# Kernel tuning notes

Measured on AMD Instinct MI355X. Metric: run time of the kernel, lower is better.

Reference implementation:

```python
import jax, jax.numpy as jnp
import numpy as np

N_NODES = 100000
N_EDGES = 3200000
NFEAT = 512
NCLASS = 10


def setup_inputs() -> dict:
    key = jax.random.key(0)
    ks = jax.random.split(key, 8)
    x = jax.random.normal(ks[0], (N_NODES, NFEAT), dtype=jnp.float32)
    edge_index = jax.random.randint(ks[1], (2, N_EDGES), 0, N_NODES, dtype=jnp.int64)
    edge_weight = jax.random.uniform(ks[2], (N_EDGES,), dtype=jnp.float32)
    def glorot(k, fan_in, fan_out):
        s = jnp.sqrt(2.0 / (fan_in + fan_out)).astype(jnp.float32)
        return jax.random.normal(k, (fan_in, fan_out), dtype=jnp.float32) * s
    W1 = glorot(ks[3], NFEAT, 8)
    W2 = glorot(ks[4], 8, 16)
    W3 = glorot(ks[5], 16, 8)
    W4 = glorot(ks[6], 8, NCLASS)
    return {
        "x": x, "edge_index": edge_index, "edge_weight": edge_weight,
        "W1": W1, "b1": jnp.zeros((8,), jnp.float32),
        "W2": W2, "b2": jnp.zeros((16,), jnp.float32),
        "W3": W3, "b3": jnp.zeros((8,), jnp.float32),
        "W4": W4, "b4": jnp.zeros((NCLASS,), jnp.float32),
    }


def gcn_conv(x, W, b, src, dst, w):
    # standard Kipf GCNConv: out = A @ (x @ W) + b, A given as weighted edge list
    h = x @ W                                   # [N, F_out]  (tiny F_out)
    msg = h[src] * w[:, None]                   # gather + scale  [E, F_out]
    agg = jax.ops.segment_sum(msg, dst, num_segments=x.shape[0])
    return agg + b


def reference(x, edge_index, edge_weight, W1, b1, W2, b2, W3, b3, W4, b4):
    src, dst = edge_index[0], edge_index[1]
    # dropout is a no-op in eval mode (training=False)
    h = jax.nn.relu(gcn_conv(x, W1, b1, src, dst, edge_weight))
    h = jax.nn.relu(gcn_conv(h, W2, b2, src, dst, edge_weight))
    h = jax.nn.relu(gcn_conv(h, W3, b3, src, dst, edge_weight))
    h = gcn_conv(h, W4, b4, src, dst, edge_weight)
    return jax.nn.log_softmax(h, axis=1)
```

## Files before the change

### kernel.cpp

```cpp
#include <hip/hip_runtime.h>
#include <hip/hip_bf16.h>
#include <math.h>

#define NFEAT 512
#define SCAN_BS 256

__global__ __launch_bounds__(256) void gcn_mm512x8(
    const float* __restrict__ x, const float* __restrict__ W,
    float* __restrict__ out, int N)
{
  const int lane   = threadIdx.x & 63;
  const int wid    = blockIdx.x * (blockDim.x >> 6) + (threadIdx.x >> 6);
  const int nwaves = gridDim.x * (blockDim.x >> 6);

  float Wr[8][8];
  #pragma unroll
  for (int k = 0; k < 8; ++k) {
    const float4 wa = *reinterpret_cast<const float4*>(W + (size_t)(lane*8 + k)*8);
    const float4 wb = *reinterpret_cast<const float4*>(W + (size_t)(lane*8 + k)*8 + 4);
    Wr[k][0]=wa.x; Wr[k][1]=wa.y; Wr[k][2]=wa.z; Wr[k][3]=wa.w;
    Wr[k][4]=wb.x; Wr[k][5]=wb.y; Wr[k][6]=wb.z; Wr[k][7]=wb.w;
  }

  for (int n = wid; n < N; n += nwaves) {
    const float* xr = x + (size_t)n * NFEAT + lane*8;
    const float4 a0 = *reinterpret_cast<const float4*>(xr);
    const float4 a1 = *reinterpret_cast<const float4*>(xr + 4);
    const float a[8] = {a0.x,a0.y,a0.z,a0.w,a1.x,a1.y,a1.z,a1.w};
    float acc[8] = {0.f,0.f,0.f,0.f,0.f,0.f,0.f,0.f};
    #pragma unroll
    for (int k = 0; k < 8; ++k)
      #pragma unroll
      for (int o = 0; o < 8; ++o)
        acc[o] = fmaf(a[k], Wr[k][o], acc[o]);
    #pragma unroll
    for (int o = 0; o < 8; ++o) {
      float v = acc[o];
      v += __shfl_xor(v, 32, 64); v += __shfl_xor(v, 16, 64);
      v += __shfl_xor(v,  8, 64); v += __shfl_xor(v,  4, 64);
      v += __shfl_xor(v,  2, 64); v += __shfl_xor(v,  1, 64);
      acc[o] = v;
    }
    if (lane == 0) {
      float4* op = reinterpret_cast<float4*>(out + (size_t)n*8);
      op[0] = make_float4(acc[0],acc[1],acc[2],acc[3]);
      op[1] = make_float4(acc[4],acc[5],acc[6],acc[7]);
    }
  }
}

__global__ __launch_bounds__(256) void gcn_hist_rank(
    const int* __restrict__ dst, int* __restrict__ deg,
    int* __restrict__ rank, int E)
{
  const int e = blockIdx.x * blockDim.x + threadIdx.x;
  if (e < E) rank[e] = atomicAdd(&deg[dst[e]], 1);
}

__global__ __launch_bounds__(SCAN_BS) void gcn_scan_block(
    const int* __restrict__ deg, int* __restrict__ exc,
    int* __restrict__ bsums, int N)
{
  __shared__ int sm[SCAN_BS];
  const int i = blockIdx.x * SCAN_BS + threadIdx.x;
  const int v = (i < N) ? deg[i] : 0;
  sm[threadIdx.x] = v;
  __syncthreads();
  for (int off = 1; off < SCAN_BS; off <<= 1) {
    const int t = (threadIdx.x >= off) ? sm[threadIdx.x - off] : 0;
    __syncthreads();
    sm[threadIdx.x] += t;
    __syncthreads();
  }
  if (i < N) exc[i] = sm[threadIdx.x] - v;
  if (threadIdx.x == SCAN_BS-1) bsums[blockIdx.x] = sm[threadIdx.x];
}

__global__ __launch_bounds__(1024) void gcn_scan_bsums(int* __restrict__ bsums, int NB)
{
  __shared__ int sm[1024];
  const int t = threadIdx.x;
  const int v = (t < NB) ? bsums[t] : 0;
  sm[t] = v;
  __syncthreads();
  for (int off = 1; off < 1024; off <<= 1) {
    const int u = (t >= off) ? sm[t - off] : 0;
    __syncthreads();
    sm[t] += u;
    __syncthreads();
  }
  if (t < NB) bsums[t] = sm[t] - v;
}

__global__ __launch_bounds__(SCAN_BS) void gcn_scan_add(
    int* __restrict__ exc, const int* __restrict__ bsums, int N)
{
  const int i = blockIdx.x * SCAN_BS + threadIdx.x;
  if (i < N) exc[i] += bsums[blockIdx.x];
}

__global__ __launch_bounds__(256) void gcn_csr_scatter(
    const int* __restrict__ src, const int* __restrict__ dst,
    const float* __restrict__ w, const int* __restrict__ rowoff,
    const int* __restrict__ rank, int2* __restrict__ csr, int E)
{
  const int e = blockIdx.x * blockDim.x + threadIdx.x;
  if (e >= E) return;
  const int pos = rowoff[dst[e]] + rank[e];
  const unsigned long long payload =
      (unsigned long long)(unsigned)src[e] |
      ((unsigned long long)(unsigned)__float_as_int(w[e]) << 32);
  __builtin_nontemporal_store(payload, (unsigned long long*)&csr[pos]);
}

template<int FIN, int FOUT>
__global__ __launch_bounds__(256) void gcn_agg_layer(
    const int* __restrict__ rowoff, const int2* __restrict__ csr,
    const float* __restrict__ hin,
    const float* __restrict__ bias, const float* __restrict__ W,
    float* __restrict__ hout, int N, int E)
{
  const int sub = threadIdx.x & 15;
  const int n   = (blockIdx.x * blockDim.x + threadIdx.x) >> 4;
  if (n >= N) return;
  const int beg = rowoff[n];
  const int end = (n + 1 < N) ? rowoff[n + 1] : E;

  float acc[FIN];
  #pragma unroll
  for (int k = 0; k < FIN; ++k) acc[k] = 0.f;

  for (int e = beg + sub; e < end; e += 16) {
    const int2  sw = csr[e];
    const float wt = __int_as_float(sw.y);
    const float* hp = hin + (size_t)sw.x * FIN;
    if constexpr ((FIN & 3) == 0) {
      #pragma unroll
      for (int q = 0; q < FIN/4; ++q) {
        const float4 v = reinterpret_cast<const float4*>(hp)[q];
        acc[q*4+0] = fmaf(v.x, wt, acc[q*4+0]);
        acc[q*4+1] = fmaf(v.y, wt, acc[q*4+1]);
        acc[q*4+2] = fmaf(v.z, wt, acc[q*4+2]);
        acc[q*4+3] = fmaf(v.w, wt, acc[q*4+3]);
      }
    } else {
      #pragma unroll
      for (int q = 0; q < FIN/2; ++q) {
        const float2 v = reinterpret_cast<const float2*>(hp)[q];
        acc[q*2+0] = fmaf(v.x, wt, acc[q*2+0]);
        acc[q*2+1] = fmaf(v.y, wt, acc[q*2+1]);
      }
    }
  }
  #pragma unroll
  for (int k = 0; k < FIN; ++k) {
    float v = acc[k];
    v += __shfl_xor(v, 8, 64); v += __shfl_xor(v, 4, 64);
    v += __shfl_xor(v, 2, 64); v += __shfl_xor(v, 1, 64);
    acc[k] = v;
  }
  #pragma unroll
  for (int k = 0; k < FIN; ++k) {
    const float t = acc[k] + bias[k];
    acc[k] = t > 0.f ? t : 0.f;
  }
  if (sub < FOUT) {
    float o = 0.f;
    #pragma unroll
    for (int k = 0; k < FIN; ++k)
      o = fmaf(acc[k], W[k*FOUT + sub], o);
    hout[(size_t)n*FOUT + sub] = o;
  }
}

__global__ __launch_bounds__(256) void gcn_agg_final(
    const int* __restrict__ rowoff, const int2* __restrict__ csr,
    const float* __restrict__ hin,
    const float* __restrict__ bias, float* __restrict__ out, int N, int E)
{
  const int sub = threadIdx.x & 15;
  const int n   = (blockIdx.x * blockDim.x + threadIdx.x) >> 4;
  if (n >= N) return;
  const int beg = rowoff[n];
  const int end = (n + 1 < N) ? rowoff[n + 1] : E;

  float acc[10];
  #pragma unroll
  for (int k = 0; k < 10; ++k) acc[k] = 0.f;

  for (int e = beg + sub; e < end; e += 16) {
    const int2  sw = csr[e];
    const float wt = __int_as_float(sw.y);
    const float* hp = hin + (size_t)sw.x * 10;
    #pragma unroll
    for (int q = 0; q < 5; ++q) {
      const float2 v = reinterpret_cast<const float2*>(hp)[q];
      acc[q*2+0] = fmaf(v.x, wt, acc[q*2+0]);
      acc[q*2+1] = fmaf(v.y, wt, acc[q*2+1]);
    }
  }
  #pragma unroll
  for (int k = 0; k < 10; ++k) {
    float v = acc[k];
    v += __shfl_xor(v, 8, 64); v += __shfl_xor(v, 4, 64);
    v += __shfl_xor(v, 2, 64); v += __shfl_xor(v, 1, 64);
    acc[k] = v + bias[k];
  }
  float m = acc[0];
  #pragma unroll
  for (int k = 1; k < 10; ++k) m = fmaxf(m, acc[k]);
  float s = 0.f;
  #pragma unroll
  for (int k = 0; k < 10; ++k) s += expf(acc[k] - m);
  const float ls = logf(s) + m;
  if (sub < 10)
    out[(size_t)n*10 + sub] = acc[sub] - ls;
}

extern "C" void kernel_launch(void* const* d_in, const int* in_sizes, int n_in,
                              void* d_out, int out_size, void* d_ws, size_t ws_size,
                              hipStream_t stream)
{
  const float* x  = (const float*)d_in[0];
  const int*   ei = (const int*)  d_in[1];
  const float* ew = (const float*)d_in[2];
  const float* W1 = (const float*)d_in[3];
  const float* b1 = (const float*)d_in[4];
  const float* W2 = (const float*)d_in[5];
  const float* b2 = (const float*)d_in[6];
  const float* W3 = (const float*)d_in[7];
  const float* b3 = (const float*)d_in[8];
  const float* W4 = (const float*)d_in[9];
  const float* b4 = (const float*)d_in[10];

  const int N = in_sizes[0] / NFEAT;
  const int E = in_sizes[2];
  const int* src = ei;
  const int* dst = ei + E;

  const int NB = (N + SCAN_BS - 1) / SCAN_BS;

  int*   wsp    = (int*)d_ws;
  int*   deg    = wsp;
  int*   rowoff = wsp + N;
  int*   bsums  = wsp + 2*(size_t)N;
  int*   rank   = wsp + 2*(size_t)N + 1024;
  int2*  csr    = (int2*)(rank + E);
  float* h8     = (float*)(csr + E);
  float* h16    = h8 + (size_t)N*8;
  float* h10    = h16;
  float* outp   = (float*)d_out;

  const int eb   = (E + 255) / 256;
  const int nb16 = (N*16 + 255) / 256;

  hipMemsetAsync(deg, 0, (size_t)N*sizeof(int), stream);
  gcn_hist_rank<<<eb, 256, 0, stream>>>(dst, deg, rank, E);
  gcn_scan_block<<<NB, SCAN_BS, 0, stream>>>(deg, rowoff, bsums, N);
  gcn_scan_bsums<<<1, 1024, 0, stream>>>(bsums, NB);
  gcn_scan_add<<<NB, SCAN_BS, 0, stream>>>(rowoff, bsums, N);
  gcn_csr_scatter<<<eb, 256, 0, stream>>>(src, dst, ew, rowoff, rank, csr, E);

  gcn_mm512x8<<<2048, 256, 0, stream>>>(x, W1, h8, N);

  gcn_agg_layer<8,16><<<nb16, 256, 0, stream>>>(rowoff, csr, h8,  b1, W2, h16, N, E);
  gcn_agg_layer<16,8><<<nb16, 256, 0, stream>>>(rowoff, csr, h16, b2, W3, h8,  N, E);
  gcn_agg_layer<8,10><<<nb16, 256, 0, stream>>>(rowoff, csr, h8,  b3, W4, h10, N, E);
  gcn_agg_final<<<nb16, 256, 0, stream>>>(rowoff, csr, h10, b4, outp, N, E);
}
```

Measured before the change: 714.1 us.

## Build CSR via two-pass bucketed partition to localize scatter writes

Replaces the single random scatter of edges into CSR with a two-pass scheme. The first pass partitions edges into coarse destination buckets of 1024 nodes using a shared-memory histogram and per-bucket global cursors. The second pass places each bucketed edge at its final CSR slot, with workgroups mapped so each XCD handles a contiguous range. The aim is to make the final scatter writes land in a narrow address window, improving cache and write locality, at the cost of an extra read/write pass over the edges and more workspace. It falls back to the old path if the workspace is too small or there are more than 128 buckets.

```diff
diff --git a/kernel.cpp b/kernel.cpp
--- a/kernel.cpp
+++ b/kernel.cpp
@@ -4,6 +4,8 @@
 
 #define NFEAT 512
 #define SCAN_BS 256
+#define PART_ITER 8
+#define BUCK_SHIFT 10
 
 __global__ __launch_bounds__(256) void gcn_mm512x8(
     const float* __restrict__ x, const float* __restrict__ W,
@@ -97,6 +99,67 @@
 {
   const int i = blockIdx.x * SCAN_BS + threadIdx.x;
   if (i < N) exc[i] += bsums[blockIdx.x];
+}
+
+__global__ void gcn_bucket_init(const int* __restrict__ rowoff,
+                                int* __restrict__ gcur, int NBUCK)
+{
+  const int b = blockIdx.x * blockDim.x + threadIdx.x;
+  if (b < NBUCK) gcur[b] = rowoff[b << BUCK_SHIFT];
+}
+
+__global__ __launch_bounds__(256) void gcn_partition(
+    const int* __restrict__ src, const int* __restrict__ dst,
+    const float* __restrict__ w, const int* __restrict__ rowoff,
+    const int* __restrict__ rank, int* __restrict__ gcur,
+    int* __restrict__ spos, int2* __restrict__ spay, int E)
+{
+  __shared__ int hist[128], base[128];
+  const int tid = threadIdx.x;
+  if (tid < 128) hist[tid] = 0;
+  __syncthreads();
+
+  const int e0 = blockIdx.x * (256 * PART_ITER);
+  int d[PART_ITER], b[PART_ITER], lr[PART_ITER];
+  #pragma unroll
+  for (int j = 0; j < PART_ITER; ++j) {
+    const int e = e0 + j*256 + tid;
+    if (e < E) {
+      d[j]  = dst[e];
+      b[j]  = d[j] >> BUCK_SHIFT;
+      lr[j] = atomicAdd(&hist[b[j]], 1);
+    }
+  }
+  __syncthreads();
+  if (tid < 128) {
+    const int c = hist[tid];
+    base[tid] = c ? atomicAdd(&gcur[tid], c) : 0;
+  }
+  __syncthreads();
+  #pragma unroll
+  for (int j = 0; j < PART_ITER; ++j) {
+    const int e = e0 + j*256 + tid;
+    if (e < E) {
+      const int slot = base[b[j]] + lr[j];
+      spos[slot] = rowoff[d[j]] + rank[e];
+      spay[slot] = make_int2(src[e], __float_as_int(w[e]));
+    }
+  }
+}
+
+__global__ __launch_bounds__(256) void gcn_place(
+    const int* __restrict__ spos, const int2* __restrict__ spay,
+    int2* __restrict__ csr, int E, int nwg)
+{
+  const int q = nwg >> 3, r = nwg & 7;
+  const int xcd = blockIdx.x & 7, i = blockIdx.x >> 3;
+  const int lb = (xcd < r) ? (xcd*(q+1) + i) : (r*(q+1) + (xcd - r)*q + i);
+  const int e0 = lb * (256 * PART_ITER);
+  #pragma unroll
+  for (int j = 0; j < PART_ITER; ++j) {
+    const int s = e0 + j*256 + threadIdx.x;
+    if (s < E) csr[spos[s]] = spay[s];
+  }
 }
 
 __global__ __launch_bounds__(256) void gcn_csr_scatter(
@@ -238,33 +301,68 @@
   const int* src = ei;
   const int* dst = ei + E;
 
-  const int NB = (N + SCAN_BS - 1) / SCAN_BS;
-
-  int*   wsp    = (int*)d_ws;
-  int*   deg    = wsp;
-  int*   rowoff = wsp + N;
-  int*   bsums  = wsp + 2*(size_t)N;
-  int*   rank   = wsp + 2*(size_t)N + 1024;
-  int2*  csr    = (int2*)(rank + E);
-  float* h8     = (float*)(csr + E);
-  float* h16    = h8 + (size_t)N*8;
-  float* h10    = h16;
-  float* outp   = (float*)d_out;
+  const int NB    = (N + SCAN_BS - 1) / SCAN_BS;
+  const int NBUCK = (N + (1 << BUCK_SHIFT) - 1) >> BUCK_SHIFT;
 
   const int eb   = (E + 255) / 256;
   const int nb16 = (N*16 + 255) / 256;
-
-  hipMemsetAsync(deg, 0, (size_t)N*sizeof(int), stream);
-  gcn_hist_rank<<<eb, 256, 0, stream>>>(dst, deg, rank, E);
-  gcn_scan_block<<<NB, SCAN_BS, 0, stream>>>(deg, rowoff, bsums, N);
-  gcn_scan_bsums<<<1, 1024, 0, stream>>>(bsums, NB);
-  gcn_scan_add<<<NB, SCAN_BS, 0, stream>>>(rowoff, bsums, N);
-  gcn_csr_scatter<<<eb, 256, 0, stream>>>(src, dst, ew, rowoff, rank, csr, E);
-
-  gcn_mm512x8<<<2048, 256, 0, stream>>>(x, W1, h8, N);
-
-  gcn_agg_layer<8,16><<<nb16, 256, 0, stream>>>(rowoff, csr, h8,  b1, W2, h16, N, E);
-  gcn_agg_layer<16,8><<<nb16, 256, 0, stream>>>(rowoff, csr, h16, b2, W3, h8,  N, E);
-  gcn_agg_layer<8,10><<<nb16, 256, 0, stream>>>(rowoff, csr, h8,  b3, W4, h10, N, E);
-  gcn_agg_final<<<nb16, 256, 0, stream>>>(rowoff, csr, h10, b4, outp, N, E);
-}
+  const int pb   = (E + 256*PART_ITER - 1) / (256*PART_ITER);
+
+  const size_t need2 = ((size_t)2*N + 1024 + 256 + 6*(size_t)E) * 4;
+  const bool twopass = (ws_size >= need2) && (NBUCK <= 128);
+
+  int* wsp = (int*)d_ws;
+  if (twopass) {
+    int*   deg    = wsp;
+    int*   rowoff = wsp + N;
+    int*   bsums  = wsp + 2*(size_t)N;
+    int*   gcur   = bsums + 1024;
+    int*   rank   = gcur + 256;
+    int*   spos   = rank + E;
+    int2*  spay   = (int2*)(spos + E);
+    int2*  csr    = spay + E;
+    float* h8     = (float*)spos;
+    float* h16    = (float*)spay;
+    float* h10    = h16;
+    float* outp   = (float*)d_out;
+
+    hipMemsetAsync(deg, 0, (size_t)N*sizeof(int), stream);
+    gcn_hist_rank<<<eb, 256, 0, stream>>>(dst, deg, rank, E);
+    gcn_scan_block<<<NB, SCAN_BS, 0, stream>>>(deg, rowoff, bsums, N);
+    gcn_scan_bsums<<<1, 1024, 0, stream>>>(bsums, NB);
+    gcn_scan_add<<<NB, SCAN_BS, 0, stream>>>(rowoff, bsums, N);
+    gcn_bucket_init<<<1, 128, 0, stream>>>(rowoff, gcur, NBUCK);
+    gcn_partition<<<pb, 256, 0, stream>>>(src, dst, ew, rowoff, rank, gcur,
+                                          spos, spay, E);
+    gcn_place<<<pb, 256, 0, stream>>>(spos, spay, csr, E, pb);
+
+    gcn_mm512x8<<<2048, 256, 0, stream>>>(x, W1, h8, N);
+    gcn_agg_layer<8,16><<<nb16, 256, 0, stream>>>(rowoff, csr, h8,  b1, W2, h16, N, E);
+    gcn_agg_layer<16,8><<<nb16, 256, 0, stream>>>(rowoff, csr, h16, b2, W3, h8,  N, E);
+    gcn_agg_layer<8,10><<<nb16, 256, 0, stream>>>(rowoff, csr, h8,  b3, W4, h10, N, E);
+    gcn_agg_final<<<nb16, 256, 0, stream>>>(rowoff, csr, h10, b4, outp, N, E);
+  } else {
+    int*   deg    = wsp;
+    int*   rowoff = wsp + N;
+    int*   bsums  = wsp + 2*(size_t)N;
+    int*   rank   = wsp + 2*(size_t)N + 1024;
+    int2*  csr    = (int2*)(rank + E);
+    float* h8     = (float*)(csr + E);
+    float* h16    = h8 + (size_t)N*8;
+    float* h10    = h16;
+    float* outp   = (float*)d_out;
+
+    hipMemsetAsync(deg, 0, (size_t)N*sizeof(int), stream);
+    gcn_hist_rank<<<eb, 256, 0, stream>>>(dst, deg, rank, E);
+    gcn_scan_block<<<NB, SCAN_BS, 0, stream>>>(deg, rowoff, bsums, N);
+    gcn_scan_bsums<<<1, 1024, 0, stream>>>(bsums, NB);
+    gcn_scan_add<<<NB, SCAN_BS, 0, stream>>>(rowoff, bsums, N);
+    gcn_csr_scatter<<<eb, 256, 0, stream>>>(src, dst, ew, rowoff, rank, csr, E);
+
+    gcn_mm512x8<<<2048, 256, 0, stream>>>(x, W1, h8, N);
+    gcn_agg_layer<8,16><<<nb16, 256, 0, stream>>>(rowoff, csr, h8,  b1, W2, h16, N, E);
+    gcn_agg_layer<16,8><<<nb16, 256, 0, stream>>>(rowoff, csr, h16, b2, W3, h8,  N, E);
+    gcn_agg_layer<8,10><<<nb16, 256, 0, stream>>>(rowoff, csr, h8,  b3, W4, h10, N, E);
+    gcn_agg_final<<<nb16, 256, 0, stream>>>(rowoff, csr, h10, b4, outp, N, E);
+  }
+}
```

Result: no change. 720.0 us (+0.8%).

## Build CSR via two-level bucket partition with shared-memory atomics

Applied to the files above, without the earlier changes.

Replaces the per-edge global atomic histogram, multi-kernel scan and random scatter with a coarse bucket partition by destination (512 nodes per bucket) followed by a per-bucket block that builds row offsets and CSR entries using shared-memory atomics. The source index and local destination are packed into one int to stage edges compactly. This aims to cut contended global atomics and scattered writes, at the cost of an extra staging pass and a workspace-size requirement. A fallback path keeps the old build when conditions are not met.

```diff
diff --git a/kernel.cpp b/kernel.cpp
--- a/kernel.cpp
+++ b/kernel.cpp
@@ -4,6 +4,10 @@
 
 #define NFEAT 512
 #define SCAN_BS 256
+#define PART_ITER 16
+#define BUCK_SHIFT 9
+#define SRC_BITS 17
+#define SRC_MASK ((1 << SRC_BITS) - 1)
 
 __global__ __launch_bounds__(256) void gcn_mm512x8(
     const float* __restrict__ x, const float* __restrict__ W,
@@ -46,6 +50,114 @@
       op[0] = make_float4(acc[0],acc[1],acc[2],acc[3]);
       op[1] = make_float4(acc[4],acc[5],acc[6],acc[7]);
     }
+  }
+}
+
+__global__ __launch_bounds__(256) void gcn_bucket_count(
+    const int* __restrict__ dst, int* __restrict__ bcnt, int E, int NBUCK)
+{
+  __shared__ int h[256];
+  const int tid = threadIdx.x;
+  h[tid] = 0;
+  __syncthreads();
+  const int e0 = blockIdx.x * (256 * PART_ITER);
+  #pragma unroll
+  for (int j = 0; j < PART_ITER; ++j) {
+    const int e = e0 + j*256 + tid;
+    if (e < E) atomicAdd(&h[dst[e] >> BUCK_SHIFT], 1);
+  }
+  __syncthreads();
+  if (tid < NBUCK && h[tid]) atomicAdd(&bcnt[tid], h[tid]);
+}
+
+__global__ __launch_bounds__(256) void gcn_bucket_scan(
+    const int* __restrict__ bcnt, int* __restrict__ bbase,
+    int* __restrict__ gcur, int NBUCK, int E)
+{
+  __shared__ int sm[256];
+  const int t = threadIdx.x;
+  const int v = (t < NBUCK) ? bcnt[t] : 0;
+  sm[t] = v;
+  __syncthreads();
+  for (int off = 1; off < 256; off <<= 1) {
+    const int u = (t >= off) ? sm[t - off] : 0;
+    __syncthreads();
+    sm[t] += u;
+    __syncthreads();
+  }
+  if (t < NBUCK) { bbase[t] = sm[t] - v; gcur[t] = sm[t] - v; }
+  if (t == NBUCK) bbase[NBUCK] = E;
+}
+
+__global__ __launch_bounds__(256) void gcn_partition(
+    const int* __restrict__ src, const int* __restrict__ dst,
+    const float* __restrict__ w, int* __restrict__ gcur,
+    int2* __restrict__ staged, int E, int NBUCK)
+{
+  __shared__ int hist[256], base[256];
+  const int tid = threadIdx.x;
+  hist[tid] = 0;
+  __syncthreads();
+  const int e0 = blockIdx.x * (256 * PART_ITER);
+  int b_[PART_ITER], lr_[PART_ITER];
+  #pragma unroll
+  for (int j = 0; j < PART_ITER; ++j) {
+    const int e = e0 + j*256 + tid;
+    if (e < E) {
+      b_[j]  = dst[e] >> BUCK_SHIFT;
+      lr_[j] = atomicAdd(&hist[b_[j]], 1);
+    }
+  }
+  __syncthreads();
+  if (tid < NBUCK) {
+    const int c = hist[tid];
+    base[tid] = c ? atomicAdd(&gcur[tid], c) : 0;
+  }
+  __syncthreads();
+  #pragma unroll
+  for (int j = 0; j < PART_ITER; ++j) {
+    const int e = e0 + j*256 + tid;
+    if (e < E) {
+      const int dl = dst[e] & ((1 << BUCK_SHIFT) - 1);
+      staged[base[b_[j]] + lr_[j]] =
+          make_int2((dl << SRC_BITS) | src[e], __float_as_int(w[e]));
+    }
+  }
+}
+
+__global__ __launch_bounds__(512) void gcn_build(
+    const int2* __restrict__ staged, const int* __restrict__ bbase,
+    int* __restrict__ rowoff, int2* __restrict__ csr, int N)
+{
+  __shared__ int h[512];
+  __shared__ int cur[512];
+  const int tid  = threadIdx.x;
+  const int b    = blockIdx.x;
+  const int base = bbase[b];
+  const int cnt  = bbase[b + 1] - base;
+
+  h[tid] = 0;
+  __syncthreads();
+  for (int s = tid; s < cnt; s += 512)
+    atomicAdd(&h[staged[base + s].x >> SRC_BITS], 1);
+  __syncthreads();
+  const int v = h[tid];
+  for (int off = 1; off < 512; off <<= 1) {
+    const int u = (tid >= off) ? h[tid - off] : 0;
+    __syncthreads();
+    h[tid] += u;
+    __syncthreads();
+  }
+  const int excl = h[tid] - v;
+  const int node = (b << BUCK_SHIFT) + tid;
+  if (node < N) rowoff[node] = base + excl;
+  cur[tid] = excl;
+  __syncthreads();
+  for (int s = tid; s < cnt; s += 512) {
+    const int2 kv  = staged[base + s];
+    const int  dl  = kv.x >> SRC_BITS;
+    const int slot = atomicAdd(&cur[dl], 1);
+    csr[base + slot] = make_int2(kv.x & SRC_MASK, kv.y);
   }
 }
 
@@ -238,33 +350,64 @@
   const int* src = ei;
   const int* dst = ei + E;
 
-  const int NB = (N + SCAN_BS - 1) / SCAN_BS;
-
-  int*   wsp    = (int*)d_ws;
-  int*   deg    = wsp;
-  int*   rowoff = wsp + N;
-  int*   bsums  = wsp + 2*(size_t)N;
-  int*   rank   = wsp + 2*(size_t)N + 1024;
-  int2*  csr    = (int2*)(rank + E);
-  float* h8     = (float*)(csr + E);
-  float* h16    = h8 + (size_t)N*8;
-  float* h10    = h16;
-  float* outp   = (float*)d_out;
-
-  const int eb   = (E + 255) / 256;
-  const int nb16 = (N*16 + 255) / 256;
-
-  hipMemsetAsync(deg, 0, (size_t)N*sizeof(int), stream);
-  gcn_hist_rank<<<eb, 256, 0, stream>>>(dst, deg, rank, E);
-  gcn_scan_block<<<NB, SCAN_BS, 0, stream>>>(deg, rowoff, bsums, N);
-  gcn_scan_bsums<<<1, 1024, 0, stream>>>(bsums, NB);
-  gcn_scan_add<<<NB, SCAN_BS, 0, stream>>>(rowoff, bsums, N);
-  gcn_csr_scatter<<<eb, 256, 0, stream>>>(src, dst, ew, rowoff, rank, csr, E);
-
-  gcn_mm512x8<<<2048, 256, 0, stream>>>(x, W1, h8, N);
-
-  gcn_agg_layer<8,16><<<nb16, 256, 0, stream>>>(rowoff, csr, h8,  b1, W2, h16, N, E);
-  gcn_agg_layer<16,8><<<nb16, 256, 0, stream>>>(rowoff, csr, h16, b2, W3, h8,  N, E);
-  gcn_agg_layer<8,10><<<nb16, 256, 0, stream>>>(rowoff, csr, h8,  b3, W4, h10, N, E);
-  gcn_agg_final<<<nb16, 256, 0, stream>>>(rowoff, csr, h10, b4, outp, N, E);
-}
+  const int NBUCK = (N + (1 << BUCK_SHIFT) - 1) >> BUCK_SHIFT;
+  const int eb    = (E + 255) / 256;
+  const int nb16  = (N*16 + 255) / 256;
+  const int pb    = (E + 256*PART_ITER - 1) / (256*PART_ITER);
+
+  int* wsp = (int*)d_ws;
+
+  const size_t S     = 768 + (size_t)N;
+  const size_t need2 = (S + 4*(size_t)E) * 4;
+  const bool binned  = (ws_size >= need2) && (N <= (1 << SRC_BITS)) &&
+                       (NBUCK < 256) && ((N & 1) == 0);
+
+  if (binned) {
+    int*   bcnt   = wsp;
+    int*   bbase  = wsp + 256;
+    int*   gcur   = wsp + 512;
+    int*   rowoff = wsp + 768;
+    int2*  staged = (int2*)(wsp + S);
+    int2*  csr    = staged + E;
+    float* h8     = (float*)staged;
+    float* h16    = h8 + (size_t)N*8;
+    float* h10    = h16;
+    float* outp   = (float*)d_out;
+
+    hipMemsetAsync(bcnt, 0, 256*sizeof(int), stream);
+    gcn_bucket_count<<<pb, 256, 0, stream>>>(dst, bcnt, E, NBUCK);
+    gcn_bucket_scan<<<1, 256, 0, stream>>>(bcnt, bbase, gcur, NBUCK, E);
+    gcn_partition<<<pb, 256, 0, stream>>>(src, dst, ew, gcur, staged, E, NBUCK);
+    gcn_build<<<NBUCK, 512, 0, stream>>>(staged, bbase, rowoff, csr, N);
+
+    gcn_mm512x8<<<2048, 256, 0, stream>>>(x, W1, h8, N);
+    gcn_agg_layer<8,16><<<nb16, 256, 0, stream>>>(rowoff, csr, h8,  b1, W2, h16, N, E);
+    gcn_agg_layer<16,8><<<nb16, 256, 0, stream>>>(rowoff, csr, h16, b2, W3, h8,  N, E);
+    gcn_agg_layer<8,10><<<nb16, 256, 0, stream>>>(rowoff, csr, h8,  b3, W4, h10, N, E);
+    gcn_agg_final<<<nb16, 256, 0, stream>>>(rowoff, csr, h10, b4, outp, N, E);
+  } else {
+    const int NB = (N + SCAN_BS - 1) / SCAN_BS;
+    int*   deg    = wsp;
+    int*   rowoff = wsp + N;
+    int*   bsums  = wsp + 2*(size_t)N;
+    int*   rank   = wsp + 2*(size_t)N + 1024;
+    int2*  csr    = (int2*)(rank + E);
+    float* h8     = (float*)(csr + E);
+    float* h16    = h8 + (size_t)N*8;
+    float* h10    = h16;
+    float* outp   = (float*)d_out;
+
+    hipMemsetAsync(deg, 0, (size_t)N*sizeof(int), stream);
+    gcn_hist_rank<<<eb, 256, 0, stream>>>(dst, deg, rank, E);
+    gcn_scan_block<<<NB, SCAN_BS, 0, stream>>>(deg, rowoff, bsums, N);
+    gcn_scan_bsums<<<1, 1024, 0, stream>>>(bsums, NB);
+    gcn_scan_add<<<NB, SCAN_BS, 0, stream>>>(rowoff, bsums, N);
+    gcn_csr_scatter<<<eb, 256, 0, stream>>>(src, dst, ew, rowoff, rank, csr, E);
+
+    gcn_mm512x8<<<2048, 256, 0, stream>>>(x, W1, h8, N);
+    gcn_agg_layer<8,16><<<nb16, 256, 0, stream>>>(rowoff, csr, h8,  b1, W2, h16, N, E);
+    gcn_agg_layer<16,8><<<nb16, 256, 0, stream>>>(rowoff, csr, h16, b2, W3, h8,  N, E);
+    gcn_agg_layer<8,10><<<nb16, 256, 0, stream>>>(rowoff, csr, h8,  b3, W4, h10, N, E);
+    gcn_agg_final<<<nb16, 256, 0, stream>>>(rowoff, csr, h10, b4, outp, N, E);
+  }
+}
```

Result: faster. 573.1 us (-19.7%).
